# Optimization experiments

Hardware: AMD Instinct MI355X
Metric: run time of the kernel (lower is better)

## Reference

```python
import jax, jax.numpy as jnp
import numpy as np

L = 6          # n_layers
D = 128        # patch_dim
COND = 128     # cond_dim
HID = 256      # hidden (fixed default in AffineCoupling)
DIN = D // 2 + COND  # 192, input dim of coupling net


def setup_inputs() -> dict:
    key = jax.random.key(0)
    ks = jax.random.split(key, 8)
    x = jax.random.normal(ks[0], (512, 128, D), dtype=jnp.float32)
    cond = jax.random.normal(ks[1], (512, COND), dtype=jnp.float32)
    # per-layer weights stacked over L; stored [in, out] (torch Linear transposed)
    W1 = jax.random.normal(ks[2], (L, DIN, HID), dtype=jnp.float32) * 0.05
    b1 = jnp.zeros((L, HID), dtype=jnp.float32)
    W2 = jax.random.normal(ks[3], (L, HID, HID), dtype=jnp.float32) * 0.05
    b2 = jnp.zeros((L, HID), dtype=jnp.float32)
    W3 = jax.random.normal(ks[4], (L, HID, D), dtype=jnp.float32) * 0.05
    b3 = jnp.zeros((L, D), dtype=jnp.float32)
    return {"x": x, "cond": cond, "W1": W1, "b1": b1, "W2": W2, "b2": b2, "W3": W3, "b3": b3}


def reference(x, cond, W1, b1, W2, b2, W3, b3):
    B, P, Dd = x.shape
    # cond is shared across patches: broadcast to [B, P, COND]
    condb = jnp.broadcast_to(cond[:, None, :], (B, P, cond.shape[-1]))
    z = x
    logdet = jnp.zeros((B,), dtype=x.dtype)
    for i in range(W1.shape[0]):
        x1, x2 = jnp.split(z, 2, axis=-1)                       # [B,P,D/2] each
        h = jnp.concatenate([x1, condb], axis=-1)               # [B,P,DIN]
        h = jax.nn.relu(jnp.einsum('bpi,ih->bph', h, W1[i]) + b1[i])
        h = jax.nn.relu(jnp.einsum('bph,hk->bpk', h, W2[i]) + b2[i])
        st = jnp.einsum('bpk,kd->bpd', h, W3[i]) + b3[i]        # [B,P,D]
        s, t = jnp.split(st, 2, axis=-1)
        s = jnp.tanh(s) * 0.5
        y2 = x2 * jnp.exp(s) + t
        z = jnp.concatenate([x1, y2], axis=-1)[..., ::-1]        # flip feature dim
        logdet = logdet + s.sum(axis=(1, 2))
    return z, logdet
```

## Files before the change

### kernel.cpp

```cpp
#include <hip/hip_runtime.h>
#include <stdint.h>

#define NLAYERS 6
#define DD      128
#define CONDD   128
#define HID     256
#define DIN     192
#define TM      32
#define NTHR    256
#define SA      72
#define SB      264

typedef __attribute__((ext_vector_type(4))) float f32x4;
typedef __attribute__((ext_vector_type(8))) short short8;

#define G1_KS 2
#define G2_KS 8
#define G3_KS 8
#define G1_FR (G1_KS*16)
#define G2_FR (G2_KS*16)
#define G3_FR (G3_KS*8)
#define FR_L  (G1_FR+G2_FR+G3_FR)
#define EL_L  (FR_L*512)
#define G2_OFF (G1_FR*512)
#define G3_OFF ((G1_FR+G2_FR)*512)

__device__ __forceinline__ short f2bf(float f) {
  uint32_t u = __builtin_bit_cast(uint32_t, f);
  u += 0x7fffu + ((u >> 16) & 1u);
  return (short)(u >> 16);
}
__device__ __forceinline__ uint32_t cvtpk(float lo, float hi) {
  uint32_t r;
  asm("v_cvt_pk_bf16_f32 %0, %1, %2" : "=v"(r) : "v"(lo), "v"(hi));
  return r;
}
__device__ __forceinline__ int kinv(int p) {
  return (p & ~63) | (p & 32) | ((p & 1) << 4) | ((p >> 1) & 15);
}

__global__ void prep_weights(const float* __restrict__ W1,
                             const float* __restrict__ W2,
                             const float* __restrict__ W3,
                             short* __restrict__ wp)
{
  int t = blockIdx.x * 256 + threadIdx.x;
  int lay  = t / (FR_L * 64);
  int rem  = t - lay * (FR_L * 64);
  int frag = rem >> 6;
  int lane = rem & 63;
  const float* src;
  int N, f2, dstbase, nfr, perm;
  if (frag < G1_FR) {
    f2 = frag;                  src = W1 + (size_t)lay * DIN * HID; N = HID; dstbase = 0;      nfr = 16; perm = 0;
  } else if (frag < G1_FR + G2_FR) {
    f2 = frag - G1_FR;          src = W2 + (size_t)lay * HID * HID; N = HID; dstbase = G2_OFF; nfr = 16; perm = 1;
  } else {
    f2 = frag - (G1_FR + G2_FR);src = W3 + (size_t)lay * HID * DD;  N = DD;  dstbase = G3_OFF; nfr = 8;  perm = 2;
  }
  int ks = f2 / nfr, nf = f2 - ks * nfr;
  int lv = lane & 15;
  int n;
  if (perm == 2) {
    int g = nf >> 1, h = nf & 1;
    int c = 16 * g + lv;
    if (lay & 1) c = 63 - c;
    n = c + 64 * h;
  } else {
    n = nf * 16 + lv;
  }
  int k0 = ks * 32 + (lane >> 4) * 8;
  short8 v;
#pragma unroll
  for (int j = 0; j < 8; ++j) {
    int k = perm ? kinv(k0 + j) : (k0 + j);
    v[j] = f2bf(src[(size_t)k * N + n]);
  }
  *(short8*)(wp + (size_t)lay * EL_L + dstbase + ((size_t)f2 * 64 + lane) * 8) = v;
}

__global__ void prep_c1(const float* __restrict__ cond, const float* __restrict__ W1,
                        const float* __restrict__ b1, float* __restrict__ c1)
{
  int lay = blockIdx.x >> 9;
  int b   = blockIdx.x & 511;
  int h   = threadIdx.x;
  const float* wb = W1 + (size_t)lay * DIN * HID + 64 * HID + h;
  const float* cb = cond + b * CONDD;
  float acc = b1[lay * HID + h];
#pragma unroll 4
  for (int c = 0; c < CONDD; ++c) acc = fmaf(cb[c], wb[(size_t)c * HID], acc);
  c1[((size_t)lay * 512 + b) * HID + h] = acc;
}

__global__ __launch_bounds__(NTHR, 4)
void flow_kernel(const float* __restrict__ x,
                 const float* __restrict__ c1g, const float* __restrict__ b2g,
                 const float* __restrict__ b3g, const short* __restrict__ wp,
                 float* __restrict__ outz, float* __restrict__ outld)
{
  __shared__ alignas(16) short bufA[TM * SA];
  __shared__ alignas(16) short bufB[TM * SB];
  __shared__ alignas(16) short bufC[TM * SB];
  __shared__ float red[4];

  const int tid  = threadIdx.x;
  const int wave = tid >> 6;
  const int lane = tid & 63;
  const int l15  = lane & 15;
  const int l4   = lane >> 4;
  const int nq   = wave;
  const int t0   = blockIdx.x * TM;
  const int batch = t0 >> 7;

  const int cB = 16 * nq + l15;
  const int rbase = 4 * l4;
  float zlo[8], zhi[8];
  {
    const float* xb = x + (size_t)t0 * DD;
#pragma unroll
    for (int m2 = 0; m2 < 2; ++m2)
#pragma unroll
      for (int r = 0; r < 4; ++r) {
        int j = m2 * 4 + r;
        int row = rbase + 16 * m2 + r;
        zlo[j] = xb[row * DD + cB];
        zhi[j] = xb[row * DD + 64 + cB];
      }
#pragma unroll
    for (int m2 = 0; m2 < 2; ++m2)
#pragma unroll
      for (int r = 0; r < 4; ++r) {
        int row = rbase + 16 * m2 + r;
        bufA[row * SA + cB] = f2bf(zlo[m2 * 4 + r]);
      }
  }
  float ldsum = 0.f;
  __syncthreads();

#pragma unroll 1
  for (int lay = 0; lay < NLAYERS; ++lay) {
    const short* wl = wp + (size_t)lay * EL_L;
    const int cl = (lay & 1) ? (63 - cB) : cB;

    {
      const float* c1row = c1g + ((size_t)lay * 512 + batch) * HID;
      f32x4 acc[2][4];
#pragma unroll
      for (int nf = 0; nf < 4; ++nf) {
        float b = c1row[64 * nq + 16 * nf + l15];
        f32x4 bi = {b, b, b, b};
        acc[0][nf] = bi; acc[1][nf] = bi;
      }
#pragma unroll 1
      for (int ks = 0; ks < G1_KS; ++ks) {
        short8 bb[4];
#pragma unroll
        for (int nf = 0; nf < 4; ++nf)
          bb[nf] = *(const short8*)(wl + (((ks * 16 + 4 * nq + nf) * 64 + lane) * 8));
#pragma unroll
        for (int m2 = 0; m2 < 2; ++m2) {
          int row = 16 * m2 + l15;
          short8 a = *(const short8*)(bufA + row * SA + ks * 32 + l4 * 8);
#pragma unroll
          for (int nf = 0; nf < 4; ++nf)
            acc[m2][nf] = __builtin_amdgcn_mfma_f32_16x16x32_bf16(a, bb[nf], acc[m2][nf], 0, 0, 0);
        }
      }
#pragma unroll
      for (int h = 0; h < 2; ++h)
#pragma unroll
        for (int m2 = 0; m2 < 2; ++m2)
#pragma unroll
          for (int r = 0; r < 4; ++r) {
            int row = rbase + 16 * m2 + r;
            float v0 = fmaxf(acc[m2][2 * h][r], 0.f);
            float v1 = fmaxf(acc[m2][2 * h + 1][r], 0.f);
            *(uint32_t*)(bufB + row * SB + 64 * nq + 32 * h + 2 * l15) = cvtpk(v0, v1);
          }
    }
    __syncthreads();

    {
      const short* wg = wl + G2_OFF;
      f32x4 acc[2][4];
#pragma unroll
      for (int nf = 0; nf < 4; ++nf) {
        float b = b2g[lay * HID + 64 * nq + 16 * nf + l15];
        f32x4 bi = {b, b, b, b};
        acc[0][nf] = bi; acc[1][nf] = bi;
      }
#pragma unroll 2
      for (int ks = 0; ks < G2_KS; ++ks) {
        short8 bb[4];
#pragma unroll
        for (int nf = 0; nf < 4; ++nf)
          bb[nf] = *(const short8*)(wg + (((ks * 16 + 4 * nq + nf) * 64 + lane) * 8));
#pragma unroll
        for (int m2 = 0; m2 < 2; ++m2) {
          int row = 16 * m2 + l15;
          short8 a = *(const short8*)(bufB + row * SB + ks * 32 + l4 * 8);
#pragma unroll
          for (int nf = 0; nf < 4; ++nf)
            acc[m2][nf] = __builtin_amdgcn_mfma_f32_16x16x32_bf16(a, bb[nf], acc[m2][nf], 0, 0, 0);
        }
      }
#pragma unroll
      for (int h = 0; h < 2; ++h)
#pragma unroll
        for (int m2 = 0; m2 < 2; ++m2)
#pragma unroll
          for (int r = 0; r < 4; ++r) {
            int row = rbase + 16 * m2 + r;
            float v0 = fmaxf(acc[m2][2 * h][r], 0.f);
            float v1 = fmaxf(acc[m2][2 * h + 1][r], 0.f);
            *(uint32_t*)(bufC + row * SB + 64 * nq + 32 * h + 2 * l15) = cvtpk(v0, v1);
          }
    }
    __syncthreads();

    {
      f32x4 acc3[2][2];
      {
        float bs = b3g[lay * DD + cl];
        float bt = b3g[lay * DD + 64 + cl];
        f32x4 bsi = {bs, bs, bs, bs}, bti = {bt, bt, bt, bt};
        acc3[0][0] = bsi; acc3[1][0] = bsi;
        acc3[0][1] = bti; acc3[1][1] = bti;
      }
#pragma unroll 2
      for (int ks = 0; ks < G3_KS; ++ks) {
        short8 bb[2];
#pragma unroll
        for (int nf = 0; nf < 2; ++nf)
          bb[nf] = *(const short8*)(wl + G3_OFF + (((ks * 8 + 2 * nq + nf) * 64 + lane) * 8));
#pragma unroll
        for (int m2 = 0; m2 < 2; ++m2) {
          int row = 16 * m2 + l15;
          short8 a = *(const short8*)(bufC + row * SB + ks * 32 + l4 * 8);
          acc3[m2][0] = __builtin_amdgcn_mfma_f32_16x16x32_bf16(a, bb[0], acc3[m2][0], 0, 0, 0);
          acc3[m2][1] = __builtin_amdgcn_mfma_f32_16x16x32_bf16(a, bb[1], acc3[m2][1], 0, 0, 0);
        }
      }
#pragma unroll
      for (int m2 = 0; m2 < 2; ++m2)
#pragma unroll
        for (int r = 0; r < 4; ++r) {
          int j = m2 * 4 + r;
          float sr = fminf(fmaxf(acc3[m2][0][r], -8.f), 8.f);
          float tt = acc3[m2][1][r];
          float e2 = __expf(2.f * sr);
          float s  = 0.5f * (e2 - 1.f) / (e2 + 1.f);
          ldsum += s;
          float y2 = fmaf(zhi[j], __expf(s), tt);
          zhi[j] = zlo[j];
          zlo[j] = y2;
        }
      if (lay < NLAYERS - 1) {
        int cn = 63 - cl;
#pragma unroll
        for (int m2 = 0; m2 < 2; ++m2)
#pragma unroll
          for (int r = 0; r < 4; ++r) {
            int row = rbase + 16 * m2 + r;
            bufA[row * SA + cn] = f2bf(zlo[m2 * 4 + r]);
          }
        __syncthreads();
      }
    }
  }

  {
    float* ob = outz + (size_t)t0 * DD;
#pragma unroll
    for (int m2 = 0; m2 < 2; ++m2)
#pragma unroll
      for (int r = 0; r < 4; ++r) {
        int j = m2 * 4 + r;
        int row = rbase + 16 * m2 + r;
        ob[row * DD + cB]      = zlo[j];
        ob[row * DD + 64 + cB] = zhi[j];
      }
  }
#pragma unroll
  for (int off = 32; off > 0; off >>= 1) ldsum += __shfl_down(ldsum, off);
  if (lane == 0) red[wave] = ldsum;
  __syncthreads();
  if (tid == 0) {
    float s = red[0] + red[1] + red[2] + red[3];
    atomicAdd(&outld[batch], s);
  }
}

extern "C" void kernel_launch(void* const* d_in, const int* in_sizes, int n_in,
                              void* d_out, int out_size, void* d_ws, size_t ws_size,
                              hipStream_t stream)
{
  (void)in_sizes; (void)n_in; (void)out_size; (void)ws_size;
  const float* x   = (const float*)d_in[0];
  const float* cnd = (const float*)d_in[1];
  const float* W1  = (const float*)d_in[2];
  const float* b1  = (const float*)d_in[3];
  const float* W2  = (const float*)d_in[4];
  const float* b2  = (const float*)d_in[5];
  const float* W3  = (const float*)d_in[6];
  const float* b3  = (const float*)d_in[7];
  float* outz  = (float*)d_out;
  float* outld = outz + (size_t)512 * 128 * 128;
  short* wp = (short*)d_ws;
  float* c1 = (float*)((char*)d_ws + (2u << 20));

  hipMemsetAsync(outld, 0, 512 * sizeof(float), stream);
  prep_weights<<<336, 256, 0, stream>>>(W1, W2, W3, wp);
  prep_c1<<<6 * 512, 256, 0, stream>>>(cnd, W1, b1, c1);
  flow_kernel<<<2048, NTHR, 0, stream>>>(x, c1, b2, b3, wp, outz, outld);
}
```

Baseline: 159.7 us.

## Prefetch next weight fragments across stages and widen hidden-activation LDS stores

Weight fragments for each GEMM stage are software-pipelined: the first k-slice of the next stage (and of the next layer's first GEMM) is loaded before the barrier, and inside the K loops the next slice is loaded while the current one feeds MFMAs. This hides global/L2 weight load latency behind compute and barriers. The K-permutation of W2/W3 is changed (kinv2) so each lane can write four packed bf16 hidden values as one 64-bit LDS store instead of two 32-bit stores. In exchange it uses more registers, which could lower occupancy, and it relies on the new permutation staying consistent between the prep and main kernels.

```diff
diff --git a/kernel.cpp b/kernel.cpp
--- a/kernel.cpp
+++ b/kernel.cpp
@@ -13,6 +13,7 @@
 
 typedef __attribute__((ext_vector_type(4))) float f32x4;
 typedef __attribute__((ext_vector_type(8))) short short8;
+typedef __attribute__((ext_vector_type(2))) uint32_t u32x2;
 
 #define G1_KS 2
 #define G2_KS 8
@@ -35,8 +36,8 @@
   asm("v_cvt_pk_bf16_f32 %0, %1, %2" : "=v"(r) : "v"(lo), "v"(hi));
   return r;
 }
-__device__ __forceinline__ int kinv(int p) {
-  return (p & ~63) | (p & 32) | ((p & 1) << 4) | ((p >> 1) & 15);
+__device__ __forceinline__ int kinv2(int p) {
+  return (p & ~63) | ((p & 3) << 4) | ((p >> 2) & 15);
 }
 
 __global__ void prep_weights(const float* __restrict__ W1,
@@ -73,7 +74,7 @@
   short8 v;
 #pragma unroll
   for (int j = 0; j < 8; ++j) {
-    int k = perm ? kinv(k0 + j) : (k0 + j);
+    int k = perm ? kinv2(k0 + j) : (k0 + j);
     v[j] = f2bf(src[(size_t)k * N + n]);
   }
   *(short8*)(wp + (size_t)lay * EL_L + dstbase + ((size_t)f2 * 64 + lane) * 8) = v;
@@ -116,6 +117,7 @@
   const int cB = 16 * nq + l15;
   const int rbase = 4 * l4;
   float zlo[8], zhi[8];
+  short8 g1pre[4];
   {
     const float* xb = x + (size_t)t0 * DD;
 #pragma unroll
@@ -134,6 +136,9 @@
         int row = rbase + 16 * m2 + r;
         bufA[row * SA + cB] = f2bf(zlo[m2 * 4 + r]);
       }
+#pragma unroll
+    for (int nf = 0; nf < 4; ++nf)
+      g1pre[nf] = *(const short8*)(wp + (((4 * nq + nf) * 64 + lane) * 8));
   }
   float ldsum = 0.f;
   __syncthreads();
@@ -142,6 +147,7 @@
   for (int lay = 0; lay < NLAYERS; ++lay) {
     const short* wl = wp + (size_t)lay * EL_L;
     const int cl = (lay & 1) ? (63 - cB) : cB;
+    short8 g2pre[4], g3pre[2];
 
     {
       const float* c1row = c1g + ((size_t)lay * 512 + batch) * HID;
@@ -152,32 +158,38 @@
         f32x4 bi = {b, b, b, b};
         acc[0][nf] = bi; acc[1][nf] = bi;
       }
-#pragma unroll 1
-      for (int ks = 0; ks < G1_KS; ++ks) {
-        short8 bb[4];
+      short8 nb1[4];
+#pragma unroll
+      for (int nf = 0; nf < 4; ++nf)
+        nb1[nf] = *(const short8*)(wl + (((16 + 4 * nq + nf) * 64 + lane) * 8));
+#pragma unroll
+      for (int m2 = 0; m2 < 2; ++m2) {
+        int row = 16 * m2 + l15;
+        short8 a = *(const short8*)(bufA + row * SA + l4 * 8);
 #pragma unroll
         for (int nf = 0; nf < 4; ++nf)
-          bb[nf] = *(const short8*)(wl + (((ks * 16 + 4 * nq + nf) * 64 + lane) * 8));
-#pragma unroll
-        for (int m2 = 0; m2 < 2; ++m2) {
-          int row = 16 * m2 + l15;
-          short8 a = *(const short8*)(bufA + row * SA + ks * 32 + l4 * 8);
-#pragma unroll
-          for (int nf = 0; nf < 4; ++nf)
-            acc[m2][nf] = __builtin_amdgcn_mfma_f32_16x16x32_bf16(a, bb[nf], acc[m2][nf], 0, 0, 0);
-        }
-      }
-#pragma unroll
-      for (int h = 0; h < 2; ++h)
-#pragma unroll
-        for (int m2 = 0; m2 < 2; ++m2)
-#pragma unroll
-          for (int r = 0; r < 4; ++r) {
-            int row = rbase + 16 * m2 + r;
-            float v0 = fmaxf(acc[m2][2 * h][r], 0.f);
-            float v1 = fmaxf(acc[m2][2 * h + 1][r], 0.f);
-            *(uint32_t*)(bufB + row * SB + 64 * nq + 32 * h + 2 * l15) = cvtpk(v0, v1);
-          }
+          acc[m2][nf] = __builtin_amdgcn_mfma_f32_16x16x32_bf16(a, g1pre[nf], acc[m2][nf], 0, 0, 0);
+      }
+#pragma unroll
+      for (int m2 = 0; m2 < 2; ++m2) {
+        int row = 16 * m2 + l15;
+        short8 a = *(const short8*)(bufA + row * SA + 32 + l4 * 8);
+#pragma unroll
+        for (int nf = 0; nf < 4; ++nf)
+          acc[m2][nf] = __builtin_amdgcn_mfma_f32_16x16x32_bf16(a, nb1[nf], acc[m2][nf], 0, 0, 0);
+      }
+#pragma unroll
+      for (int m2 = 0; m2 < 2; ++m2)
+#pragma unroll
+        for (int r = 0; r < 4; ++r) {
+          int row = rbase + 16 * m2 + r;
+          u32x2 val = {cvtpk(fmaxf(acc[m2][0][r], 0.f), fmaxf(acc[m2][1][r], 0.f)),
+                       cvtpk(fmaxf(acc[m2][2][r], 0.f), fmaxf(acc[m2][3][r], 0.f))};
+          *(u32x2*)(bufB + row * SB + 64 * nq + 4 * l15) = val;
+        }
+#pragma unroll
+      for (int nf = 0; nf < 4; ++nf)
+        g2pre[nf] = *(const short8*)(wl + G2_OFF + (((4 * nq + nf) * 64 + lane) * 8));
     }
     __syncthreads();
 
@@ -190,12 +202,16 @@
         f32x4 bi = {b, b, b, b};
         acc[0][nf] = bi; acc[1][nf] = bi;
       }
-#pragma unroll 2
+      short8 bb[4];
+#pragma unroll
+      for (int nf = 0; nf < 4; ++nf) bb[nf] = g2pre[nf];
+#pragma unroll 1
       for (int ks = 0; ks < G2_KS; ++ks) {
-        short8 bb[4];
+        int ksn = (ks + 1 < G2_KS) ? ks + 1 : ks;
+        short8 nb[4];
 #pragma unroll
         for (int nf = 0; nf < 4; ++nf)
-          bb[nf] = *(const short8*)(wg + (((ks * 16 + 4 * nq + nf) * 64 + lane) * 8));
+          nb[nf] = *(const short8*)(wg + (((ksn * 16 + 4 * nq + nf) * 64 + lane) * 8));
 #pragma unroll
         for (int m2 = 0; m2 < 2; ++m2) {
           int row = 16 * m2 + l15;
@@ -204,18 +220,21 @@
           for (int nf = 0; nf < 4; ++nf)
             acc[m2][nf] = __builtin_amdgcn_mfma_f32_16x16x32_bf16(a, bb[nf], acc[m2][nf], 0, 0, 0);
         }
-      }
-#pragma unroll
-      for (int h = 0; h < 2; ++h)
-#pragma unroll
-        for (int m2 = 0; m2 < 2; ++m2)
-#pragma unroll
-          for (int r = 0; r < 4; ++r) {
-            int row = rbase + 16 * m2 + r;
-            float v0 = fmaxf(acc[m2][2 * h][r], 0.f);
-            float v1 = fmaxf(acc[m2][2 * h + 1][r], 0.f);
-            *(uint32_t*)(bufC + row * SB + 64 * nq + 32 * h + 2 * l15) = cvtpk(v0, v1);
-          }
+#pragma unroll
+        for (int nf = 0; nf < 4; ++nf) bb[nf] = nb[nf];
+      }
+#pragma unroll
+      for (int m2 = 0; m2 < 2; ++m2)
+#pragma unroll
+        for (int r = 0; r < 4; ++r) {
+          int row = rbase + 16 * m2 + r;
+          u32x2 val = {cvtpk(fmaxf(acc[m2][0][r], 0.f), fmaxf(acc[m2][1][r], 0.f)),
+                       cvtpk(fmaxf(acc[m2][2][r], 0.f), fmaxf(acc[m2][3][r], 0.f))};
+          *(u32x2*)(bufC + row * SB + 64 * nq + 4 * l15) = val;
+        }
+#pragma unroll
+      for (int nf = 0; nf < 2; ++nf)
+        g3pre[nf] = *(const short8*)(wl + G3_OFF + (((2 * nq + nf) * 64 + lane) * 8));
     }
     __syncthreads();
 
@@ -228,12 +247,15 @@
         acc3[0][0] = bsi; acc3[1][0] = bsi;
         acc3[0][1] = bti; acc3[1][1] = bti;
       }
-#pragma unroll 2
+      short8 bb[2];
+      bb[0] = g3pre[0]; bb[1] = g3pre[1];
+#pragma unroll 1
       for (int ks = 0; ks < G3_KS; ++ks) {
-        short8 bb[2];
+        int ksn = (ks + 1 < G3_KS) ? ks + 1 : ks;
+        short8 nb[2];
 #pragma unroll
         for (int nf = 0; nf < 2; ++nf)
-          bb[nf] = *(const short8*)(wl + G3_OFF + (((ks * 8 + 2 * nq + nf) * 64 + lane) * 8));
+          nb[nf] = *(const short8*)(wl + G3_OFF + (((ksn * 8 + 2 * nq + nf) * 64 + lane) * 8));
 #pragma unroll
         for (int m2 = 0; m2 < 2; ++m2) {
           int row = 16 * m2 + l15;
@@ -241,6 +263,7 @@
           acc3[m2][0] = __builtin_amdgcn_mfma_f32_16x16x32_bf16(a, bb[0], acc3[m2][0], 0, 0, 0);
           acc3[m2][1] = __builtin_amdgcn_mfma_f32_16x16x32_bf16(a, bb[1], acc3[m2][1], 0, 0, 0);
         }
+        bb[0] = nb[0]; bb[1] = nb[1];
       }
 #pragma unroll
       for (int m2 = 0; m2 < 2; ++m2)
@@ -257,6 +280,10 @@
           zlo[j] = y2;
         }
       if (lay < NLAYERS - 1) {
+        const short* wn = wl + EL_L;
+#pragma unroll
+        for (int nf = 0; nf < 4; ++nf)
+          g1pre[nf] = *(const short8*)(wn + (((4 * nq + nf) * 64 + lane) * 8));
         int cn = 63 - cl;
 #pragma unroll
         for (int m2 = 0; m2 < 2; ++m2)
```

Result: slower. 179.4 us (+12.4%).
